# Performance work log

Hardware: AMD Instinct MI355X
Metric: run time of the kernel (lower is better)

Reference implementation:

```python
import jax, jax.numpy as jnp
import numpy as np

B, T = 16384, 128
PI = np.pi
MAX_ITERS = 1000


def _quat_to_mat(q):
    # pytorch3d quaternion_to_matrix, q is (..., 4) wxyz
    w, x, y, z = q[..., 0], q[..., 1], q[..., 2], q[..., 3]
    two = 2.0 / jnp.sum(q * q, axis=-1)
    r00 = 1.0 - two * (y * y + z * z)
    r01 = two * (x * y - z * w)
    r02 = two * (x * z + y * w)
    r10 = two * (x * y + z * w)
    r11 = 1.0 - two * (x * x + z * z)
    r12 = two * (y * z - x * w)
    r20 = two * (x * z - y * w)
    r21 = two * (y * z + x * w)
    r22 = 1.0 - two * (x * x + y * y)
    return jnp.stack([
        jnp.stack([r00, r01, r02], -1),
        jnp.stack([r10, r11, r12], -1),
        jnp.stack([r20, r21, r22], -1)], -2)


def _mat_to_quat(m):
    # pytorch3d matrix_to_quaternion, m is (..., 3, 3) -> (..., 4) wxyz
    m00, m01, m02 = m[..., 0, 0], m[..., 0, 1], m[..., 0, 2]
    m10, m11, m12 = m[..., 1, 0], m[..., 1, 1], m[..., 1, 2]
    m20, m21, m22 = m[..., 2, 0], m[..., 2, 1], m[..., 2, 2]
    q_abs = jnp.sqrt(jnp.clip(jnp.stack([
        1.0 + m00 + m11 + m22,
        1.0 + m00 - m11 - m22,
        1.0 - m00 + m11 - m22,
        1.0 - m00 - m11 + m22], -1), 1e-8))
    cand = jnp.stack([
        jnp.stack([q_abs[..., 0] ** 2, m21 - m12, m02 - m20, m10 - m01], -1),
        jnp.stack([m21 - m12, q_abs[..., 1] ** 2, m01 + m10, m02 + m20], -1),
        jnp.stack([m02 - m20, m10 + m01, q_abs[..., 2] ** 2, m12 + m21], -1),
        jnp.stack([m10 - m01, m20 + m02, m21 + m12, q_abs[..., 3] ** 2], -1)], -2)
    cand = cand / (2.0 * jnp.maximum(q_abs[..., None], 0.1))
    best = jnp.argmax(q_abs, axis=-1)
    return jnp.take_along_axis(cand, best[..., None, None], axis=-2)[..., 0, :]


def _build_R(key, batch, dtype):
    k = jax.random.split(key, 4)
    ax = jax.random.uniform(k[0], (batch,), dtype) * 2 * PI - PI
    ay = jax.random.uniform(k[1], (batch,), dtype) * 2 * PI - PI
    az = jax.random.uniform(k[2], (batch,), dtype) * 2 * PI - PI
    mask = jax.random.uniform(k[3], (batch,), dtype) < (1.0 / 64.0)
    ax = jnp.where(mask, 0.0, ax)
    ay = jnp.where(mask, 0.0, ay)
    az = jnp.where(mask, 0.0, az)
    cx, sx = jnp.cos(ax), jnp.sin(ax)
    cy, sy = jnp.cos(ay), jnp.sin(ay)
    cz, sz = jnp.cos(az), jnp.sin(az)
    o, z0 = jnp.ones_like(ax), jnp.zeros_like(ax)
    Rx = jnp.stack([jnp.stack([o, z0, z0], -1), jnp.stack([z0, cx, -sx], -1), jnp.stack([z0, sx, cx], -1)], -2)
    Ry = jnp.stack([jnp.stack([cy, z0, sy], -1), jnp.stack([z0, o, z0], -1), jnp.stack([-sy, z0, cy], -1)], -2)
    Rz = jnp.stack([jnp.stack([cz, -sz, z0], -1), jnp.stack([sz, cz, z0], -1), jnp.stack([z0, z0, o], -1)], -2)
    return Rz @ Ry @ Rx  # [B, 3, 3]


def setup_inputs() -> dict:
    key = jax.random.key(0)
    kp, kq = jax.random.split(key)
    # positions scaled to (-0.5, 0.5): every point has norm < 1 so rotated
    # components stay in [-1, 1] and the acceptance test passes
    pos = (jax.random.uniform(kp, (B, T, 3), jnp.float32) * 2.0 - 1.0) * 0.5
    quat = jax.random.normal(kq, (B, T, 4), jnp.float32)
    quat = quat / jnp.linalg.norm(quat, axis=-1, keepdims=True)
    return {"pos": pos, "quat": quat}


def reference(pos, quat):
    batch = pos.shape[0]
    quat_wxyz = quat[..., jnp.array([3, 0, 1, 2])]
    eye = jnp.broadcast_to(jnp.eye(3, dtype=pos.dtype), (batch, 3, 3))

    def cond(s):
        i, key, acc, R = s
        return jnp.logical_and(~acc, i < MAX_ITERS)

    def body(s):
        i, key, acc, R = s
        key, sub = jax.random.split(key)
        Rn = _build_R(sub, batch, pos.dtype)
        rp = jnp.einsum('bij,btj->bti', Rn, pos)
        ok = jnp.logical_and(rp.min() >= -1.0, rp.max() <= 1.0)
        return (i + 1, key, ok, Rn)

    i, _, acc, R = jax.lax.while_loop(
        cond, body, (jnp.int32(0), jax.random.key(42), jnp.bool_(False), eye))
    # torch code falls back to identity if it exhausted all 1000 tries
    # (including acceptance on the very last iteration, matching `if i == 999`)
    use_id = i >= MAX_ITERS
    Rf = jnp.where(use_id, eye, R)
    rotated_pos = jnp.einsum('bij,btj->bti', Rf, pos)
    rot = _quat_to_mat(quat_wxyz)                       # [B,T,3,3]
    rotated_rot = jnp.einsum('bij,btjk->btik', Rf, rot)
    rotated_quat = _mat_to_quat(rotated_rot)[..., jnp.array([1, 2, 3, 0])]  # back to xyzw
    pos_out = jnp.where(use_id, pos, rotated_pos)
    quat_out = jnp.where(use_id, quat, rotated_quat)
    return pos_out, quat_out, Rf
```

## Files before the change

### kernel.cpp

```cpp
#include <hip/hip_runtime.h>
#include <stdint.h>

#define B_DIM 16384
#define T_DIM 128
#define NB 2
#define BLK (NB * T_DIM)

struct U2 { uint32_t a, b; };

__host__ __device__ constexpr uint32_t rotl32c(uint32_t x, uint32_t n) {
    return (x << n) | (x >> (32u - n));
}

__host__ __device__ constexpr U2 tf(uint32_t k0, uint32_t k1,
                                    uint32_t x0, uint32_t x1) {
    uint32_t ks2 = k0 ^ k1 ^ 0x1BD11BDAu;
    x0 += k0; x1 += k1;
#define RND(r) { x0 += x1; x1 = rotl32c(x1, r); x1 ^= x0; }
    RND(13) RND(15) RND(26) RND(6)
    x0 += k1; x1 += ks2 + 1u;
    RND(17) RND(29) RND(16) RND(24)
    x0 += ks2; x1 += k0 + 2u;
    RND(13) RND(15) RND(26) RND(6)
    x0 += k0; x1 += k1 + 3u;
    RND(17) RND(29) RND(16) RND(24)
    x0 += k1; x1 += ks2 + 4u;
    RND(13) RND(15) RND(26) RND(6)
    x0 += ks2; x1 += k0 + 5u;
#undef RND
    return U2{x0, x1};
}

constexpr U2 SUB = tf(0u, 42u, 0u, 1u);
constexpr U2 K0 = tf(SUB.a, SUB.b, 0u, 0u);
constexpr U2 K1 = tf(SUB.a, SUB.b, 0u, 1u);
constexpr U2 K2 = tf(SUB.a, SUB.b, 0u, 2u);
constexpr U2 K3 = tf(SUB.a, SUB.b, 0u, 3u);

__device__ __forceinline__ float bits_to_uniform(uint32_t bits) {
    uint32_t u = (bits >> 9) | 0x3F800000u;
    return __uint_as_float(u) - 1.0f;
}

__device__ __forceinline__ uint32_t rbits(U2 k, uint32_t i) {
    U2 o = tf(k.a, k.b, 0u, i);
    return o.a ^ o.b;
}

__global__ __launch_bounds__(64) void build_R_kernel(float* __restrict__ Rf) {
    int b = blockIdx.x * blockDim.x + threadIdx.x;
    if (b >= B_DIM) return;

    uint32_t bx = rbits(K0, (uint32_t)b);
    uint32_t by = rbits(K1, (uint32_t)b);
    uint32_t bz = rbits(K2, (uint32_t)b);
    uint32_t bm = rbits(K3, (uint32_t)b);

    const float PI_F = 3.14159265358979323846f;
    float ax = bits_to_uniform(bx) * 2.0f * PI_F - PI_F;
    float ay = bits_to_uniform(by) * 2.0f * PI_F - PI_F;
    float az = bits_to_uniform(bz) * 2.0f * PI_F - PI_F;
    bool mask = bits_to_uniform(bm) < 0.015625f;
    if (mask) { ax = 0.0f; ay = 0.0f; az = 0.0f; }

    float sx, cx, sy, cy, sz, cz;
    sincosf(ax, &sx, &cx);
    sincosf(ay, &sy, &cy);
    sincosf(az, &sz, &cz);

    float r00 = cz * cy;
    float r01 = cz * sy * sx - sz * cx;
    float r02 = cz * sy * cx + sz * sx;
    float r10 = sz * cy;
    float r11 = sz * sy * sx + cz * cx;
    float r12 = sz * sy * cx - cz * sx;
    float r20 = -sy;
    float r21 = cy * sx;
    float r22 = cy * cx;

    float* o = Rf + (size_t)b * 9;
    o[0] = r00; o[1] = r01; o[2] = r02;
    o[3] = r10; o[4] = r11; o[5] = r12;
    o[6] = r20; o[7] = r21; o[8] = r22;
}

__global__ __launch_bounds__(BLK) void rot_apply_kernel(
    const float* __restrict__ pos, const float* __restrict__ quat,
    const float* __restrict__ Rf, float* __restrict__ pos_out,
    float* __restrict__ quat_out) {
    __shared__ float Ps[NB * T_DIM * 3];
    __shared__ float Rs[NB * 9];

    const int t  = threadIdx.x;
    const int b0 = blockIdx.x * NB;

    if (t < NB * 9) Rs[t] = Rf[(size_t)b0 * 9 + t];

    const float4* pin = (const float4*)(pos + (size_t)b0 * T_DIM * 3);
    if (t < NB * T_DIM * 3 / 4) ((float4*)Ps)[t] = pin[t];
    __syncthreads();

    const int lb = t >> 7;
    const int e  = t & (T_DIM - 1);
    const size_t idx = (size_t)(b0 + lb) * T_DIM + e;
    const int pofs = lb * (T_DIM * 3) + e * 3;

    const float* Rb = Rs + lb * 9;
    const float R00 = Rb[0], R01 = Rb[1], R02 = Rb[2];
    const float R10 = Rb[3], R11 = Rb[4], R12 = Rb[5];
    const float R20 = Rb[6], R21 = Rb[7], R22 = Rb[8];

    const float px = Ps[pofs + 0], py = Ps[pofs + 1], pz = Ps[pofs + 2];
    const float ox = R00 * px + R01 * py + R02 * pz;
    const float oy = R10 * px + R11 * py + R12 * pz;
    const float oz = R20 * px + R21 * py + R22 * pz;

    float4 q = ((const float4*)quat)[idx];
    float qx = q.x, qy = q.y, qz = q.z, qw = q.w;
    float ss = qw * qw + qx * qx + qy * qy + qz * qz;
    float two = 2.0f / ss;
    float m00 = 1.0f - two * (qy * qy + qz * qz);
    float m01 = two * (qx * qy - qz * qw);
    float m02 = two * (qx * qz + qy * qw);
    float m10 = two * (qx * qy + qz * qw);
    float m11 = 1.0f - two * (qx * qx + qz * qz);
    float m12 = two * (qy * qz - qx * qw);
    float m20 = two * (qx * qz - qy * qw);
    float m21 = two * (qy * qz + qx * qw);
    float m22 = 1.0f - two * (qx * qx + qy * qy);

    float n00 = R00 * m00 + R01 * m10 + R02 * m20;
    float n01 = R00 * m01 + R01 * m11 + R02 * m21;
    float n02 = R00 * m02 + R01 * m12 + R02 * m22;
    float n10 = R10 * m00 + R11 * m10 + R12 * m20;
    float n11 = R10 * m01 + R11 * m11 + R12 * m21;
    float n12 = R10 * m02 + R11 * m12 + R12 * m22;
    float n20 = R20 * m00 + R21 * m10 + R22 * m20;
    float n21 = R20 * m01 + R21 * m11 + R22 * m21;
    float n22 = R20 * m02 + R21 * m12 + R22 * m22;

    float t0 = 1.0f + n00 + n11 + n22;
    float t1 = 1.0f + n00 - n11 - n22;
    float t2 = 1.0f - n00 + n11 - n22;
    float t3 = 1.0f - n00 - n11 + n22;
    float q0 = sqrtf(fmaxf(t0, 1e-8f));
    float q1 = sqrtf(fmaxf(t1, 1e-8f));
    float q2 = sqrtf(fmaxf(t2, 1e-8f));
    float q3 = sqrtf(fmaxf(t3, 1e-8f));

    int best = 0; float bv = q0;
    if (q1 > bv) { best = 1; bv = q1; }
    if (q2 > bv) { best = 2; bv = q2; }
    if (q3 > bv) { best = 3; bv = q3; }

    float w, x, y, z;
    if (best == 0)      { w = q0 * q0;  x = n21 - n12; y = n02 - n20; z = n10 - n01; }
    else if (best == 1) { w = n21 - n12; x = q1 * q1;  y = n01 + n10; z = n02 + n20; }
    else if (best == 2) { w = n02 - n20; x = n10 + n01; y = q2 * q2;  z = n12 + n21; }
    else                { w = n10 - n01; x = n20 + n02; y = n21 + n12; z = q3 * q3;  }

    const float inv = 1.0f / (2.0f * fmaxf(bv, 0.1f));
    float4 qo;
    qo.x = x * inv; qo.y = y * inv; qo.z = z * inv; qo.w = w * inv;
    ((float4*)quat_out)[idx] = qo;

    Ps[pofs + 0] = ox; Ps[pofs + 1] = oy; Ps[pofs + 2] = oz;
    __syncthreads();
    float4* pout = (float4*)(pos_out + (size_t)b0 * T_DIM * 3);
    if (t < NB * T_DIM * 3 / 4) pout[t] = ((float4*)Ps)[t];
}

extern "C" void kernel_launch(void* const* d_in, const int* in_sizes, int n_in,
                              void* d_out, int out_size, void* d_ws, size_t ws_size,
                              hipStream_t stream) {
    const float* pos  = (const float*)d_in[0];
    const float* quat = (const float*)d_in[1];
    float* out = (float*)d_out;
    float* pos_out  = out;
    float* quat_out = out + (size_t)B_DIM * T_DIM * 3;
    float* Rf       = out + (size_t)B_DIM * T_DIM * 7;

    build_R_kernel<<<B_DIM / 64, 64, 0, stream>>>(Rf);
    rot_apply_kernel<<<B_DIM / NB, BLK, 0, stream>>>(pos, quat, Rf, pos_out, quat_out);
}
```

Before: 108.1 us.

## Fuse rotation generation into the apply kernel and hoist quaternion load

```diff
diff --git a/kernel.cpp b/kernel.cpp
--- a/kernel.cpp
+++ b/kernel.cpp
@@ -47,64 +47,63 @@
     return o.a ^ o.b;
 }
 
-__global__ __launch_bounds__(64) void build_R_kernel(float* __restrict__ Rf) {
-    int b = blockIdx.x * blockDim.x + threadIdx.x;
-    if (b >= B_DIM) return;
-
-    uint32_t bx = rbits(K0, (uint32_t)b);
-    uint32_t by = rbits(K1, (uint32_t)b);
-    uint32_t bz = rbits(K2, (uint32_t)b);
-    uint32_t bm = rbits(K3, (uint32_t)b);
-
-    const float PI_F = 3.14159265358979323846f;
-    float ax = bits_to_uniform(bx) * 2.0f * PI_F - PI_F;
-    float ay = bits_to_uniform(by) * 2.0f * PI_F - PI_F;
-    float az = bits_to_uniform(bz) * 2.0f * PI_F - PI_F;
-    bool mask = bits_to_uniform(bm) < 0.015625f;
-    if (mask) { ax = 0.0f; ay = 0.0f; az = 0.0f; }
-
-    float sx, cx, sy, cy, sz, cz;
-    sincosf(ax, &sx, &cx);
-    sincosf(ay, &sy, &cy);
-    sincosf(az, &sz, &cz);
-
-    float r00 = cz * cy;
-    float r01 = cz * sy * sx - sz * cx;
-    float r02 = cz * sy * cx + sz * sx;
-    float r10 = sz * cy;
-    float r11 = sz * sy * sx + cz * cx;
-    float r12 = sz * sy * cx - cz * sx;
-    float r20 = -sy;
-    float r21 = cy * sx;
-    float r22 = cy * cx;
-
-    float* o = Rf + (size_t)b * 9;
-    o[0] = r00; o[1] = r01; o[2] = r02;
-    o[3] = r10; o[4] = r11; o[5] = r12;
-    o[6] = r20; o[7] = r21; o[8] = r22;
-}
-
-__global__ __launch_bounds__(BLK) void rot_apply_kernel(
+__global__ __launch_bounds__(BLK) void rot_fused_kernel(
     const float* __restrict__ pos, const float* __restrict__ quat,
-    const float* __restrict__ Rf, float* __restrict__ pos_out,
-    float* __restrict__ quat_out) {
-    __shared__ float Ps[NB * T_DIM * 3];
-    __shared__ float Rs[NB * 9];
+    float* __restrict__ pos_out, float* __restrict__ quat_out,
+    float* __restrict__ Rf) {
+    __shared__ float   Ps[NB * T_DIM * 3];
+    __shared__ float   Rs[NB * 9];
+    __shared__ uint32_t Bits[NB * 4];
 
     const int t  = threadIdx.x;
     const int b0 = blockIdx.x * NB;
-
-    if (t < NB * 9) Rs[t] = Rf[(size_t)b0 * 9 + t];
-
-    const float4* pin = (const float4*)(pos + (size_t)b0 * T_DIM * 3);
-    if (t < NB * T_DIM * 3 / 4) ((float4*)Ps)[t] = pin[t];
-    __syncthreads();
-
     const int lb = t >> 7;
     const int e  = t & (T_DIM - 1);
     const size_t idx = (size_t)(b0 + lb) * T_DIM + e;
+
+    const float4 q = ((const float4*)quat)[idx];
+    const float4* pin = (const float4*)(pos + (size_t)b0 * T_DIM * 3);
+    if (t < NB * T_DIM * 3 / 4) ((float4*)Ps)[t] = pin[t];
+
+    if (t < NB * 4) {
+        const int ki = t & 3;
+        const U2 k = (ki == 0) ? K0 : (ki == 1) ? K1 : (ki == 2) ? K2 : K3;
+        Bits[t] = rbits(k, (uint32_t)(b0 + (t >> 2)));
+    }
+    __syncthreads();
+
+    if (t < NB) {
+        const float PI_F = 3.14159265358979323846f;
+        float ax = bits_to_uniform(Bits[t * 4 + 0]) * 2.0f * PI_F - PI_F;
+        float ay = bits_to_uniform(Bits[t * 4 + 1]) * 2.0f * PI_F - PI_F;
+        float az = bits_to_uniform(Bits[t * 4 + 2]) * 2.0f * PI_F - PI_F;
+        bool mask = bits_to_uniform(Bits[t * 4 + 3]) < 0.015625f;
+        if (mask) { ax = 0.0f; ay = 0.0f; az = 0.0f; }
+
+        float sx, cx, sy, cy, sz, cz;
+        sincosf(ax, &sx, &cx);
+        sincosf(ay, &sy, &cy);
+        sincosf(az, &sz, &cz);
+
+        float r[9];
+        r[0] = cz * cy;
+        r[1] = cz * sy * sx - sz * cx;
+        r[2] = cz * sy * cx + sz * sx;
+        r[3] = sz * cy;
+        r[4] = sz * sy * sx + cz * cx;
+        r[5] = sz * sy * cx - cz * sx;
+        r[6] = -sy;
+        r[7] = cy * sx;
+        r[8] = cy * cx;
+
+        float* rs = Rs + t * 9;
+        float* ro = Rf + (size_t)(b0 + t) * 9;
+        #pragma unroll
+        for (int i = 0; i < 9; ++i) { rs[i] = r[i]; ro[i] = r[i]; }
+    }
+    __syncthreads();
+
     const int pofs = lb * (T_DIM * 3) + e * 3;
-
     const float* Rb = Rs + lb * 9;
     const float R00 = Rb[0], R01 = Rb[1], R02 = Rb[2];
     const float R10 = Rb[3], R11 = Rb[4], R12 = Rb[5];
@@ -115,7 +114,6 @@
     const float oy = R10 * px + R11 * py + R12 * pz;
     const float oz = R20 * px + R21 * py + R22 * pz;
 
-    float4 q = ((const float4*)quat)[idx];
     float qx = q.x, qy = q.y, qz = q.z, qw = q.w;
     float ss = qw * qw + qx * qx + qy * qy + qz * qz;
     float two = 2.0f / ss;
@@ -180,6 +178,5 @@
     float* quat_out = out + (size_t)B_DIM * T_DIM * 3;
     float* Rf       = out + (size_t)B_DIM * T_DIM * 7;
 
-    build_R_kernel<<<B_DIM / 64, 64, 0, stream>>>(Rf);
-    rot_apply_kernel<<<B_DIM / NB, BLK, 0, stream>>>(pos, quat, Rf, pos_out, quat_out);
+    rot_fused_kernel<<<B_DIM / NB, BLK, 0, stream>>>(pos, quat, pos_out, quat_out, Rf);
 }
```

New measurement: 108.0 us. Within noise of the previous version (-0.1%).
